# Kernel optimization log

Measured on AMD Instinct MI355X. Metric: run time of the kernel, lower is better.

Reference implementation:

```python
import jax, jax.numpy as jnp
import numpy as np

B, S, I, H = 32, 512, 1024, 1024


def _rnn_pass(x, W_ih, W_hh, b_ih, b_hh):
    # x: [B,S,I]; vanilla tanh RNN, h0 = 0. Precompute input projection once.
    xp = jnp.einsum('bsi,hi->bsh', x, W_ih) + b_ih + b_hh  # [B,S,H]
    h0 = jnp.zeros((x.shape[0], W_hh.shape[0]), dtype=x.dtype)

    def step(h, xp_t):
        h_new = jnp.tanh(xp_t + h @ W_hh.T)
        return h_new, h_new

    _, outs = jax.lax.scan(step, h0, jnp.swapaxes(xp, 0, 1))  # [S,B,H]
    return jnp.swapaxes(outs, 0, 1)  # [B,S,H]


def setup_inputs() -> dict:
    key = jax.random.key(0)
    ks = jax.random.split(key, 9)
    scale_i = 1.0 / np.sqrt(I)
    scale_h = 1.0 / np.sqrt(H)
    return {
        'x': jax.random.normal(ks[0], (B, S, I), dtype=jnp.float32),
        'W_ih_f': jax.random.normal(ks[1], (H, I), dtype=jnp.float32) * scale_i,
        'W_hh_f': jax.random.normal(ks[2], (H, H), dtype=jnp.float32) * scale_h,
        'b_ih_f': jax.random.normal(ks[3], (H,), dtype=jnp.float32) * scale_h,
        'b_hh_f': jax.random.normal(ks[4], (H,), dtype=jnp.float32) * scale_h,
        'W_ih_b': jax.random.normal(ks[5], (H, I), dtype=jnp.float32) * scale_i,
        'W_hh_b': jax.random.normal(ks[6], (H, H), dtype=jnp.float32) * scale_h,
        'b_ih_b': jax.random.normal(ks[7], (H,), dtype=jnp.float32) * scale_h,
        'b_hh_b': jax.random.normal(ks[8], (H,), dtype=jnp.float32) * scale_h,
    }


def reference(x, W_ih_f, W_hh_f, b_ih_f, b_hh_f, W_ih_b, W_hh_b, b_ih_b, b_hh_b):
    fwd = _rnn_pass(x, W_ih_f, W_hh_f, b_ih_f, b_hh_f)              # [B,S,H]
    bwd = _rnn_pass(x[:, ::-1, :], W_ih_b, W_hh_b, b_ih_b, b_hh_b)  # reversed seq
    bwd = bwd[:, ::-1, :]                                           # flip back
    return jnp.concatenate([fwd, bwd], axis=-1)  # [B,S,2H]
```

## Files before the change

kernel.cpp:

```cpp
#include <hip/hip_runtime.h>

typedef _Float16 half8  __attribute__((ext_vector_type(8)));
typedef _Float16 half4v __attribute__((ext_vector_type(4)));
typedef float    floatx4 __attribute__((ext_vector_type(4)));
typedef unsigned long long u64;

#define B_ 32
#define S_ 512
#define I_ 1024
#define H_ 1024
#define M_TOT (B_ * S_)

__global__ void cvt_f32_f16(const float* __restrict__ src, _Float16* __restrict__ dst, long n) {
  long i = ((long)blockIdx.x * blockDim.x + threadIdx.x) * 4;
  const long stride = (long)gridDim.x * blockDim.x * 4;
  for (; i < n; i += stride) {
    floatx4 v = *(const floatx4*)(src + i);
    half4v h = {(_Float16)v[0], (_Float16)v[1], (_Float16)v[2], (_Float16)v[3]};
    *(half4v*)(dst + i) = h;
  }
}

__global__ void bias_sum_kernel(const float* __restrict__ bihf, const float* __restrict__ bhhf,
                                const float* __restrict__ bihb, const float* __restrict__ bhhb,
                                float* __restrict__ bias) {
  int i = blockIdx.x * blockDim.x + threadIdx.x;
  if (i < H_) {
    bias[i]      = bihf[i] + bhhf[i];
    bias[H_ + i] = bihb[i] + bhhb[i];
  }
}

__global__ void init_ring(unsigned int* __restrict__ hq) {
  const int i = blockIdx.x * blockDim.x + threadIdx.x;
  unsigned int v = 0u;
  if (i >= 32768) v = (i < 65536) ? 0x00020002u : 0x00010001u;
  __hip_atomic_store(hq + i, v, __ATOMIC_RELAXED, __HIP_MEMORY_SCOPE_AGENT);
}

__global__ void __launch_bounds__(256) gemm_xp_kernel(
    const _Float16* __restrict__ A,
    const _Float16* __restrict__ W,
    const float*    __restrict__ bias,
    float*          __restrict__ out)
{
  __shared__ _Float16 alds[128 * 32];
  __shared__ _Float16 blds[128 * 32];

  const int dir = blockIdx.z;
  const int m0  = blockIdx.y * 128;
  const int n0  = blockIdx.x * 128;
  const int tid  = threadIdx.x;
  const int lane = tid & 63;
  const int wv   = tid >> 6;
  const int wm   = wv >> 1, wn = wv & 1;
  const int lrow = lane & 15;
  const int lkg  = lane >> 4;

  const _Float16* Wd = W + (long)dir * H_ * I_;

  floatx4 acc[4][4] = {};

  const int srow = tid >> 1;
  const int sseg = tid & 1;

  for (int kt = 0; kt < 32; ++kt) {
    __syncthreads();
    {
      const _Float16* srcA = A  + (long)(m0 + srow) * I_ + kt * 32 + sseg * 16;
      const _Float16* srcB = Wd + (long)(n0 + srow) * I_ + kt * 32 + sseg * 16;
      half8 a0 = *(const half8*)(srcA);
      half8 a1 = *(const half8*)(srcA + 8);
      half8 b0 = *(const half8*)(srcB);
      half8 b1 = *(const half8*)(srcB + 8);
      const int sw = (srow & 7) << 4;
      const int base = srow * 64 + sseg * 32;
      *(half8*)((char*)alds + ((base     ) ^ sw)) = a0;
      *(half8*)((char*)alds + ((base + 16) ^ sw)) = a1;
      *(half8*)((char*)blds + ((base     ) ^ sw)) = b0;
      *(half8*)((char*)blds + ((base + 16) ^ sw)) = b1;
    }
    __syncthreads();

    half8 af[4], bf[4];
#pragma unroll
    for (int mt = 0; mt < 4; ++mt) {
      int r = wm * 64 + mt * 16 + lrow;
      int byte = (r * 64 + lkg * 16) ^ ((r & 7) << 4);
      af[mt] = *(const half8*)((const char*)alds + byte);
    }
#pragma unroll
    for (int ntt = 0; ntt < 4; ++ntt) {
      int r = wn * 64 + ntt * 16 + lrow;
      int byte = (r * 64 + lkg * 16) ^ ((r & 7) << 4);
      bf[ntt] = *(const half8*)((const char*)blds + byte);
    }
#pragma unroll
    for (int mt = 0; mt < 4; ++mt)
#pragma unroll
      for (int ntt = 0; ntt < 4; ++ntt)
        acc[mt][ntt] = __builtin_amdgcn_mfma_f32_16x16x32_f16(af[mt], bf[ntt], acc[mt][ntt], 0, 0, 0);
  }

#pragma unroll
  for (int mt = 0; mt < 4; ++mt) {
    int mrow = m0 + wm * 64 + mt * 16 + lkg * 4;
#pragma unroll
    for (int ntt = 0; ntt < 4; ++ntt) {
      int n = n0 + wn * 64 + ntt * 16 + lrow;
      float bv = bias[dir * H_ + n];
#pragma unroll
      for (int v = 0; v < 4; ++v) {
        out[(long)(mrow + v) * (2 * H_) + dir * H_ + n] = acc[mt][ntt][v] + bv;
      }
    }
  }
}

__global__ void __launch_bounds__(256, 1) scan_kernel(
    const float* __restrict__ Whh_f,
    const float* __restrict__ Whh_b,
    float*       __restrict__ out,
    _Float16*    __restrict__ hbuf)
{
  __shared__ _Float16 wlds[32 * 1024];
  __shared__ floatx4  redlds[2 * 4 * 64];

  const int w     = blockIdx.x;
  const int dir   = w >> 5;
  const int rb    = w & 31;
  const int rows0 = rb * 32;
  const float* Whh = dir ? Whh_b : Whh_f;
  const int tid = threadIdx.x;

  for (int idx = tid; idx < 32 * 128; idx += 256) {
    const int r  = idx >> 7;
    const int kg = idx & 127;
    const float* src = Whh + (long)(rows0 + r) * H_ + kg * 8;
    floatx4 v0 = *(const floatx4*)(src);
    floatx4 v1 = *(const floatx4*)(src + 4);
    half8 h = {(_Float16)v0[0], (_Float16)v0[1], (_Float16)v0[2], (_Float16)v0[3],
               (_Float16)v1[0], (_Float16)v1[1], (_Float16)v1[2], (_Float16)v1[3]};
    const int byte = (r * 2048 + kg * 16) ^ ((r & 7) << 4);
    *(half8*)((char*)wlds + byte) = h;
  }

  const int lane = tid & 63;
  const int wv   = tid >> 6;
  const int nt   = wv & 1;
  const int kh   = wv >> 1;
  const int lrow = lane & 15;
  const int lkg  = lane >> 4;
  const int b_idx = nt * 16 + lrow;
  const int kbase = kh * 512;
  const int r0    = rows0 + kh * 16 + lkg * 4;
  const int asw   = (lrow & 7) << 4;
  const int abase0 = lrow * 2048 + kbase * 2;
  const int abase1 = (16 + lrow) * 2048 + kbase * 2;

  const long hstride = (long)2 * B_ * H_;

  __syncthreads();

  long o_nxt = ((long)b_idx * S_ + (dir ? (S_ - 1) : 0)) * (2 * H_) + dir * H_ + r0;
  floatx4 xp_n = *(const floatx4*)(out + o_nxt);

  int s_in = 0;

#pragma unroll 1
  for (int t = 0; t < S_; ++t) {
    const int p = t & 1;
    const int s_out = (s_in == 2) ? 0 : (s_in + 1);

    const _Float16* hp = hbuf + (s_in * hstride) + ((long)dir * B_ + b_idx) * H_ + kbase + lkg * 8;
    const unsigned int rep = (unsigned)(t & 1) * 0x00010001u;
    half8 hr[16];
    for (;;) {
#pragma unroll
      for (int kt = 0; kt < 16; ++kt)
        asm volatile("global_load_dwordx4 %0, %1, off offset:%2 sc1"
                     : "=v"(hr[kt]) : "v"(hp), "i"(kt * 64) : "memory");
      asm volatile("s_waitcnt vmcnt(0)" ::: "memory");
      unsigned int bad = 0;
#pragma unroll
      for (int kt = 0; kt < 16; ++kt) {
        union { half8 h; unsigned int u[4]; } c; c.h = hr[kt];
        bad |= ((c.u[0] ^ rep) | (c.u[1] ^ rep) | (c.u[2] ^ rep) | (c.u[3] ^ rep))
               & 0x00010001u;
      }
      if (!__any(bad != 0)) break;
    }
    __builtin_amdgcn_sched_barrier(0);

    floatx4 a0 = {}, a1 = {};
#pragma unroll
    for (int kt = 0; kt < 16; ++kt) {
      const int koff = kt * 64 + lkg * 16;
      half8 wa = *(const half8*)((const char*)wlds + ((abase0 + koff) ^ asw));
      half8 wb = *(const half8*)((const char*)wlds + ((abase1 + koff) ^ asw));
      a0 = __builtin_amdgcn_mfma_f32_16x16x32_f16(wa, hr[kt], a0, 0, 0, 0);
      a1 = __builtin_amdgcn_mfma_f32_16x16x32_f16(wb, hr[kt], a1, 0, 0, 0);
    }

    redlds[((p * 2 + (1 - kh)) * 2 + nt) * 64 + lane] = kh ? a0 : a1;
    __syncthreads();
    floatx4 tot = (kh ? a1 : a0) + redlds[((p * 2 + kh) * 2 + nt) * 64 + lane];

    const long o = o_nxt;
    const floatx4 xpv = xp_n;
    floatx4 hv;
#pragma unroll
    for (int v = 0; v < 4; ++v) {
      float z = tot[v] + xpv[v];
      hv[v] = 1.f - 2.f / (__expf(2.f * z) + 1.f);
    }

    if (t + 1 < S_) {
      union { half4v h; u64 u; unsigned int w2[2]; } hh;
      hh.h = half4v{(_Float16)hv[0], (_Float16)hv[1], (_Float16)hv[2], (_Float16)hv[3]};
      const unsigned int eo = (unsigned)((t + 1) & 1) * 0x00010001u;
      hh.w2[0] = (hh.w2[0] & ~0x00010001u) | eo;
      hh.w2[1] = (hh.w2[1] & ~0x00010001u) | eo;
      u64* dst = (u64*)(hbuf + (s_out * hstride) + ((long)dir * B_ + b_idx) * H_ + r0);
      __hip_atomic_store(dst, hh.u, __ATOMIC_RELAXED, __HIP_MEMORY_SCOPE_AGENT);
    }

    *(floatx4*)(out + o) = hv;
    if (t + 1 < S_) {
      const int sidx1 = dir ? (S_ - 2 - t) : (t + 1);
      o_nxt = ((long)b_idx * S_ + sidx1) * (2 * H_) + dir * H_ + r0;
      xp_n = *(const floatx4*)(out + o_nxt);
    }
    s_in = s_out;
  }
}

extern "C" void kernel_launch(void* const* d_in, const int* in_sizes, int n_in,
                              void* d_out, int out_size, void* d_ws, size_t ws_size,
                              hipStream_t stream) {
  const float* x    = (const float*)d_in[0];
  const float* Wihf = (const float*)d_in[1];
  const float* Whhf = (const float*)d_in[2];
  const float* bihf = (const float*)d_in[3];
  const float* bhhf = (const float*)d_in[4];
  const float* Wihb = (const float*)d_in[5];
  const float* Whhb = (const float*)d_in[6];
  const float* bihb = (const float*)d_in[7];
  const float* bhhb = (const float*)d_in[8];
  float* out = (float*)d_out;

  char* ws = (char*)d_ws;
  _Float16*     x16  = (_Float16*)ws;
  _Float16*     w16  = (_Float16*)(ws + 33554432u);
  float*        bias = (float*)   (ws + 33554432u + 4194304u);
  _Float16*     hbuf = (_Float16*)(ws + 37756928u);

  cvt_f32_f16<<<4096, 256, 0, stream>>>(x, x16, (long)M_TOT * I_);
  cvt_f32_f16<<<1024, 256, 0, stream>>>(Wihf, w16, (long)H_ * I_);
  cvt_f32_f16<<<1024, 256, 0, stream>>>(Wihb, w16 + (long)H_ * I_, (long)H_ * I_);
  bias_sum_kernel<<<4, 256, 0, stream>>>(bihf, bhhf, bihb, bhhb, bias);
  init_ring<<<384, 256, 0, stream>>>((unsigned int*)hbuf);

  dim3 g(H_ / 128, M_TOT / 128, 2);
  gemm_xp_kernel<<<g, 256, 0, stream>>>(x16, w16, bias, out);

  void* args[] = {(void*)&Whhf, (void*)&Whhb, (void*)&out, (void*)&hbuf};
  (void)hipLaunchCooperativeKernel((void*)scan_kernel, dim3(64), dim3(256),
                                   args, 0, stream);
}
```

Baseline: 2.211 ms.

## Pin scan blocks to two XCDs and exchange hidden state via local L2

Launches 256 blocks and keeps only those with blockIdx%8 in {0,1}, so each direction's 32 blocks land on a single XCD under round-robin dispatch. Hidden state is written to both an XCD-local ring (plain store) and a device-coherent ring, and readers poll the local copy with sc0 loads. After 128 failed polls a reader falls back to the sc1 device-scope path. This aims to cut cross-die latency on the per-step handoff, but it relies on the dispatch-to-XCD mapping, on L2 coherence for plain stores, and it doubles the store traffic.

```diff
diff --git a/kernel.cpp b/kernel.cpp
--- a/kernel.cpp
+++ b/kernel.cpp
@@ -10,6 +10,8 @@
 #define I_ 1024
 #define H_ 1024
 #define M_TOT (B_ * S_)
+#define RING_HALVES (3 * 2 * B_ * H_)
+#define RING_U32    (RING_HALVES / 2)
 
 __global__ void cvt_f32_f16(const float* __restrict__ src, _Float16* __restrict__ dst, long n) {
   long i = ((long)blockIdx.x * blockDim.x + threadIdx.x) * 4;
@@ -33,8 +35,9 @@
 
 __global__ void init_ring(unsigned int* __restrict__ hq) {
   const int i = blockIdx.x * blockDim.x + threadIdx.x;
+  const int j = (i >= RING_U32) ? (i - RING_U32) : i;
   unsigned int v = 0u;
-  if (i >= 32768) v = (i < 65536) ? 0x00020002u : 0x00010001u;
+  if (j >= 32768) v = (j < 65536) ? 0x00020002u : 0x00010001u;
   __hip_atomic_store(hq + i, v, __ATOMIC_RELAXED, __HIP_MEMORY_SCOPE_AGENT);
 }
 
@@ -121,14 +124,16 @@
     const float* __restrict__ Whh_f,
     const float* __restrict__ Whh_b,
     float*       __restrict__ out,
-    _Float16*    __restrict__ hbuf)
+    _Float16*    __restrict__ hmall,
+    _Float16*    __restrict__ hloc)
 {
   __shared__ _Float16 wlds[32 * 1024];
   __shared__ floatx4  redlds[2 * 4 * 64];
 
-  const int w     = blockIdx.x;
-  const int dir   = w >> 5;
-  const int rb    = w & 31;
+  const int g = blockIdx.x & 7;
+  if (g >= 2) return;
+  const int dir = g;
+  const int rb  = blockIdx.x >> 3;
   const int rows0 = rb * 32;
   const float* Whh = dir ? Whh_b : Whh_f;
   const int tid = threadIdx.x;
@@ -159,6 +164,8 @@
   const int abase1 = (16 + lrow) * 2048 + kbase * 2;
 
   const long hstride = (long)2 * B_ * H_;
+  const long inoff_base = ((long)dir * B_ + b_idx) * H_ + kbase + lkg * 8;
+  const long outoff_base = ((long)dir * B_ + b_idx) * H_ + r0;
 
   __syncthreads();
 
@@ -166,20 +173,30 @@
   floatx4 xp_n = *(const floatx4*)(out + o_nxt);
 
   int s_in = 0;
+  int use_mall = 0;
 
 #pragma unroll 1
   for (int t = 0; t < S_; ++t) {
     const int p = t & 1;
     const int s_out = (s_in == 2) ? 0 : (s_in + 1);
 
-    const _Float16* hp = hbuf + (s_in * hstride) + ((long)dir * B_ + b_idx) * H_ + kbase + lkg * 8;
+    const _Float16* lp = hloc  + (s_in * hstride) + inoff_base;
+    const _Float16* mp = hmall + (s_in * hstride) + inoff_base;
     const unsigned int rep = (unsigned)(t & 1) * 0x00010001u;
     half8 hr[16];
+    int att = 0;
     for (;;) {
-#pragma unroll
-      for (int kt = 0; kt < 16; ++kt)
-        asm volatile("global_load_dwordx4 %0, %1, off offset:%2 sc1"
-                     : "=v"(hr[kt]) : "v"(hp), "i"(kt * 64) : "memory");
+      if (use_mall) {
+#pragma unroll
+        for (int kt = 0; kt < 16; ++kt)
+          asm volatile("global_load_dwordx4 %0, %1, off offset:%2 sc1"
+                       : "=v"(hr[kt]) : "v"(mp), "i"(kt * 64) : "memory");
+      } else {
+#pragma unroll
+        for (int kt = 0; kt < 16; ++kt)
+          asm volatile("global_load_dwordx4 %0, %1, off offset:%2 sc0"
+                       : "=v"(hr[kt]) : "v"(lp), "i"(kt * 64) : "memory");
+      }
       asm volatile("s_waitcnt vmcnt(0)" ::: "memory");
       unsigned int bad = 0;
 #pragma unroll
@@ -189,6 +206,7 @@
                & 0x00010001u;
       }
       if (!__any(bad != 0)) break;
+      if (!use_mall && (++att > 128)) use_mall = 1;
     }
     __builtin_amdgcn_sched_barrier(0);
 
@@ -221,8 +239,10 @@
       const unsigned int eo = (unsigned)((t + 1) & 1) * 0x00010001u;
       hh.w2[0] = (hh.w2[0] & ~0x00010001u) | eo;
       hh.w2[1] = (hh.w2[1] & ~0x00010001u) | eo;
-      u64* dst = (u64*)(hbuf + (s_out * hstride) + ((long)dir * B_ + b_idx) * H_ + r0);
-      __hip_atomic_store(dst, hh.u, __ATOMIC_RELAXED, __HIP_MEMORY_SCOPE_AGENT);
+      u64* dl = (u64*)(hloc  + (s_out * hstride) + outoff_base);
+      u64* dm = (u64*)(hmall + (s_out * hstride) + outoff_base);
+      asm volatile("global_store_dwordx2 %0, %1, off" :: "v"(dl), "v"(hh.u) : "memory");
+      __hip_atomic_store(dm, hh.u, __ATOMIC_RELAXED, __HIP_MEMORY_SCOPE_AGENT);
     }
 
     *(floatx4*)(out + o) = hv;
@@ -250,21 +270,22 @@
   float* out = (float*)d_out;
 
   char* ws = (char*)d_ws;
-  _Float16*     x16  = (_Float16*)ws;
-  _Float16*     w16  = (_Float16*)(ws + 33554432u);
-  float*        bias = (float*)   (ws + 33554432u + 4194304u);
-  _Float16*     hbuf = (_Float16*)(ws + 37756928u);
+  _Float16* x16   = (_Float16*)ws;
+  _Float16* w16   = (_Float16*)(ws + 33554432u);
+  float*    bias  = (float*)   (ws + 37748736u);
+  _Float16* hmall = (_Float16*)(ws + 37756928u);
+  _Float16* hloc  = (_Float16*)(ws + 38150144u);
 
   cvt_f32_f16<<<4096, 256, 0, stream>>>(x, x16, (long)M_TOT * I_);
   cvt_f32_f16<<<1024, 256, 0, stream>>>(Wihf, w16, (long)H_ * I_);
   cvt_f32_f16<<<1024, 256, 0, stream>>>(Wihb, w16 + (long)H_ * I_, (long)H_ * I_);
   bias_sum_kernel<<<4, 256, 0, stream>>>(bihf, bhhf, bihb, bhhb, bias);
-  init_ring<<<384, 256, 0, stream>>>((unsigned int*)hbuf);
+  init_ring<<<768, 256, 0, stream>>>((unsigned int*)hmall);
 
   dim3 g(H_ / 128, M_TOT / 128, 2);
   gemm_xp_kernel<<<g, 256, 0, stream>>>(x16, w16, bias, out);
 
-  void* args[] = {(void*)&Whhf, (void*)&Whhb, (void*)&out, (void*)&hbuf};
-  (void)hipLaunchCooperativeKernel((void*)scan_kernel, dim3(64), dim3(256),
+  void* args[] = {(void*)&Whhf, (void*)&Whhb, (void*)&out, (void*)&hmall, (void*)&hloc};
+  (void)hipLaunchCooperativeKernel((void*)scan_kernel, dim3(256), dim3(256),
                                    args, 0, stream);
 }
```

Result: slower. 3.084 ms (+39.5%).
